# Kernel optimization log

Measured on AMD Instinct MI355X. Metric: run time of the kernel, lower is better.

## Reference

```python
import jax, jax.numpy as jnp
import numpy as np

GROUPS = 32
HEADS = 4
EPS_GN = 1e-5
EPS_DEN = 1e-6


def group_norm(x, gamma, beta):
    b, c, h, w = x.shape
    xg = x.reshape(b, GROUPS, (c // GROUPS) * h * w)
    mu = xg.mean(axis=-1, keepdims=True)
    var = xg.var(axis=-1, keepdims=True)
    xn = ((xg - mu) * jax.lax.rsqrt(var + EPS_GN)).reshape(b, c, h, w)
    return xn * gamma[None, :, None, None] + beta[None, :, None, None]


def setup_inputs() -> dict:
    key = jax.random.key(0)
    ks = jax.random.split(key, 4)
    b, c, h, w = 16, 256, 64, 64
    x = jax.random.normal(ks[0], (b, c, h, w), dtype=jnp.float32)
    gamma = jnp.ones((c,), jnp.float32)
    beta = jnp.zeros((c,), jnp.float32)
    w_qkv = jax.random.normal(ks[1], (3 * c, c), jnp.float32) * (1.0 / np.sqrt(c))
    b_qkv = jnp.zeros((3 * c,), jnp.float32)
    w_out = jax.random.normal(ks[2], (c, c), jnp.float32) * (1.0 / np.sqrt(c))
    b_out = jnp.zeros((c,), jnp.float32)
    return {"x": x, "gamma": gamma, "beta": beta, "w_qkv": w_qkv,
            "b_qkv": b_qkv, "w_out": w_out, "b_out": b_out}


def reference(x, gamma, beta, w_qkv, b_qkv, w_out, b_out):
    b, c, h, w = x.shape
    d = c // HEADS
    n = h * w
    xn = group_norm(x, gamma, beta)
    # 1x1 conv == channel GEMM: [b,3c,h,w]
    qkv = jnp.einsum('bchw,oc->bohw', xn, w_qkv) + b_qkv[None, :, None, None]
    q, k, v = jnp.split(qkv, 3, axis=1)
    # b (heads d) h w -> b heads d n
    q = q.reshape(b, HEADS, d, n)
    k = k.reshape(b, HEADS, d, n)
    v = v.reshape(b, HEADS, d, n)
    q = jax.nn.elu(q) + 1.0
    k = jax.nn.elu(k) + 1.0
    k_sum = k.sum(axis=-1)                                 # [b,H,d]
    kv = jnp.einsum('bhdn,bhen->bhde', k, v)               # [b,H,d,d]
    out = jnp.einsum('bhde,bhdn->bhen', kv, q)             # [b,H,d,n]
    denom = jnp.einsum('bhdn,bhd->bhn', q, k_sum)          # [b,H,n]
    out = out / (denom[:, :, None, :] + EPS_DEN)
    out = out.reshape(b, c, h, w)
    out = jnp.einsum('bchw,oc->bohw', out, w_out) + b_out[None, :, None, None]
    return out + x
```

## Files before the change

kernel.cpp:

```cpp
#include <hip/hip_runtime.h>
#include <stdint.h>

#define BATCH 16
#define CH    256
#define NSP   4096
#define NH    4
#define HD    64

typedef __attribute__((ext_vector_type(8))) short bf16x8;
typedef __attribute__((ext_vector_type(4))) float f32x4;
typedef __attribute__((ext_vector_type(4))) unsigned int u32x4;

__device__ __forceinline__ short f2bf(float f) {
    union { float f; unsigned u; } v; v.f = f;
    unsigned r = (v.u + 0x7fffu + ((v.u >> 16) & 1u)) >> 16;
    return (short)r;
}
__device__ __forceinline__ float bf2f(short s) {
    union { float f; unsigned u; } v; v.u = ((unsigned)(unsigned short)s) << 16;
    return v.f;
}

__global__ __launch_bounds__(256) void k_pre(
        const float* __restrict__ x, const float* __restrict__ wq, const float* __restrict__ wo,
        const float* __restrict__ gamma, const float* __restrict__ beta,
        float* __restrict__ sc_tab, float* __restrict__ sh_tab,
        short* __restrict__ wq_bf, short* __restrict__ wo_bf) {
    int bg = blockIdx.x;
    if (bg < 512) {
        const float4* p = (const float4*)(x + (size_t)bg * 32768);
        float s = 0.f, sq = 0.f;
        #pragma unroll 4
        for (int i = threadIdx.x; i < 8192; i += 256) {
            float4 v = p[i];
            s  += v.x + v.y + v.z + v.w;
            sq += v.x * v.x + v.y * v.y + v.z * v.z + v.w * v.w;
        }
        for (int off = 32; off; off >>= 1) { s += __shfl_down(s, off); sq += __shfl_down(sq, off); }
        __shared__ float ls[4], lq[4];
        int w = threadIdx.x >> 6;
        if ((threadIdx.x & 63) == 0) { ls[w] = s; lq[w] = sq; }
        __syncthreads();
        if (threadIdx.x == 0) {
            float S = ls[0] + ls[1] + ls[2] + ls[3];
            float Q = lq[0] + lq[1] + lq[2] + lq[3];
            float m = S / 32768.f;
            float var = Q / 32768.f - m * m;
            ls[0] = m; lq[0] = rsqrtf(var + 1e-5f);
        }
        __syncthreads();
        if (threadIdx.x < 8) {
            int b = bg >> 5, g = bg & 31, c = g * 8 + threadIdx.x;
            float r = lq[0], mm = ls[0];
            float sc = r * gamma[c];
            sc_tab[b * 256 + c] = sc;
            sh_tab[b * 256 + c] = beta[c] - mm * sc;
        }
    } else {
        int idx = ((bg - 512) * 256 + threadIdx.x) * 4;
        float4 v;
        short* dst;
        if (idx < 196608) { v = *(const float4*)(wq + idx); dst = wq_bf + idx; }
        else              { v = *(const float4*)(wo + (idx - 196608)); dst = wo_bf + (idx - 196608); }
        unsigned p0 = ((unsigned)(unsigned short)f2bf(v.x)) | (((unsigned)(unsigned short)f2bf(v.y)) << 16);
        unsigned p1 = ((unsigned)(unsigned short)f2bf(v.z)) | (((unsigned)(unsigned short)f2bf(v.w)) << 16);
        uint2 pk; pk.x = p0; pk.y = p1;
        *(uint2*)dst = pk;
    }
}

__global__ __launch_bounds__(256, 3) void k_gnqkv(
        const float* __restrict__ x,
        const float* __restrict__ sc_tab, const float* __restrict__ sh_tab,
        const short* __restrict__ wq_bf, const float* __restrict__ b_qkv,
        short* __restrict__ q_t, short* __restrict__ kvp_bf, float* __restrict__ ksp) {
    int b = blockIdx.y, nt = blockIdx.x;
    int n0 = nt * 64;
    __shared__ short Blds[64 * 264];
    __shared__ union UR {
        struct { short kst[64 * 72]; short vst[64 * 72]; } s;
        short cst[64 * 136];
    } R;
    int t = threadIdx.x, lane = t & 63, wv = t >> 6, lr = lane & 15, quad = lane >> 4;

    {
        const float* xb = x + (size_t)b * CH * NSP + n0;
        const float* scb = sc_tab + b * 256;
        const float* shb = sh_tab + b * 256;
        int m = t & 15, cq = t >> 4;
        float4 vv[16];
        float scA[16], shA[16];
        #pragma unroll
        for (int cb = 0; cb < 16; cb++) {
            int c = cb * 16 + cq;
            vv[cb] = *(const float4*)(xb + (size_t)c * NSP + m * 4);
            scA[cb] = scb[c]; shA[cb] = shb[c];
        }
        #pragma unroll
        for (int cb = 0; cb < 16; cb++) {
            int c = cb * 16 + cq;
            float va[4] = {vv[cb].x, vv[cb].y, vv[cb].z, vv[cb].w};
            #pragma unroll
            for (int j = 0; j < 4; j++) {
                int n = m * 4 + j;
                int cc = c ^ (((n >> 4) & 3) << 3);
                Blds[n * 264 + cc] = f2bf(va[j] * scA[cb] + shA[cb]);
            }
        }
    }
    __syncthreads();

    #pragma unroll 1
    for (int h = 0; h < 4; h++) {
        int br0 = (wv < 2 ? 256 : 512) + h * 64;
        int sub = (wv & 1) * 32;
        bf16x8 A0[8], A1[8];
        #pragma unroll
        for (int kk = 0; kk < 8; kk++) {
            A0[kk] = *(const bf16x8*)(wq_bf + (size_t)(br0 + sub + lr) * 256 + kk * 32 + quad * 8);
            A1[kk] = *(const bf16x8*)(wq_bf + (size_t)(br0 + sub + 16 + lr) * 256 + kk * 32 + quad * 8);
        }
        __builtin_amdgcn_sched_barrier(0);
        f32x4 acc[2][4] = {};
        #pragma unroll
        for (int kk = 0; kk < 8; kk++) {
            bf16x8 bfr[4];
            #pragma unroll
            for (int ni = 0; ni < 4; ni++) {
                int rr = ni * 16 + lr;
                bfr[ni] = *(const bf16x8*)(Blds + rr * 264 + ((kk * 32 + quad * 8) ^ (((rr >> 4) & 3) << 3)));
            }
            #pragma unroll
            for (int ni = 0; ni < 4; ni++) {
                acc[0][ni] = __builtin_amdgcn_mfma_f32_16x16x32_bf16(A0[kk], bfr[ni], acc[0][ni], 0, 0, 0);
                acc[1][ni] = __builtin_amdgcn_mfma_f32_16x16x32_bf16(A1[kk], bfr[ni], acc[1][ni], 0, 0, 0);
            }
        }
        __syncthreads();
        short* dst = (wv < 2) ? R.s.kst : R.s.vst;
        bool is_k = (wv < 2);
        #pragma unroll
        for (int mi = 0; mi < 2; mi++)
          #pragma unroll
          for (int ni = 0; ni < 4; ni++)
            #pragma unroll
            for (int r = 0; r < 4; r++) {
                int ol = sub + mi * 16 + quad * 4 + r;
                int nl = ni * 16 + lr;
                float v = acc[mi][ni][r] + b_qkv[br0 + ol];
                if (is_k) v = v > 0.f ? v + 1.f : __expf(v);
                dst[ol * 72 + nl] = f2bf(v);
            }
        __syncthreads();
        {
            int d = t >> 2, nq = (t & 3) * 16;
            float s = 0.f;
            #pragma unroll
            for (int j = 0; j < 16; j++) s += bf2f(R.s.kst[d * 72 + nq + j]);
            s += __shfl_down(s, 2);
            s += __shfl_down(s, 1);
            if ((t & 3) == 0) ksp[((size_t)(b * 4 + h) * 64 + nt) * 64 + d] = s;
        }
        f32x4 acc2[4] = {};
        #pragma unroll
        for (int kk = 0; kk < 64; kk += 32) {
            bf16x8 af = *(const bf16x8*)(R.s.vst + (wv * 16 + lr) * 72 + kk + quad * 8);
            bf16x8 bfk[4];
            #pragma unroll
            for (int ni = 0; ni < 4; ni++)
                bfk[ni] = *(const bf16x8*)(R.s.kst + (ni * 16 + lr) * 72 + kk + quad * 8);
            #pragma unroll
            for (int ni = 0; ni < 4; ni++)
                acc2[ni] = __builtin_amdgcn_mfma_f32_16x16x32_bf16(af, bfk[ni], acc2[ni], 0, 0, 0);
        }
        short* kvdst = kvp_bf + ((size_t)(b * 4 + h) * 64 + nt) * 4096;
        #pragma unroll
        for (int ni = 0; ni < 4; ni++)
            #pragma unroll
            for (int r = 0; r < 4; r++)
                kvdst[(wv * 16 + quad * 4 + r) * 64 + ni * 16 + lr] = f2bf(acc2[ni][r]);
    }

    #pragma unroll 1
    for (int mtq = 0; mtq < 2; mtq++) {
        int wm = wv * 32;
        bf16x8 A0[8], A1[8];
        #pragma unroll
        for (int kk = 0; kk < 8; kk++) {
            A0[kk] = *(const bf16x8*)(wq_bf + (size_t)(mtq * 128 + wm + lr) * 256 + kk * 32 + quad * 8);
            A1[kk] = *(const bf16x8*)(wq_bf + (size_t)(mtq * 128 + wm + 16 + lr) * 256 + kk * 32 + quad * 8);
        }
        __builtin_amdgcn_sched_barrier(0);
        f32x4 acc[2][4] = {};
        #pragma unroll
        for (int kk = 0; kk < 8; kk++) {
            bf16x8 bfr[4];
            #pragma unroll
            for (int ni = 0; ni < 4; ni++) {
                int rr = ni * 16 + lr;
                bfr[ni] = *(const bf16x8*)(Blds + rr * 264 + ((kk * 32 + quad * 8) ^ (((rr >> 4) & 3) << 3)));
            }
            #pragma unroll
            for (int ni = 0; ni < 4; ni++) {
                acc[0][ni] = __builtin_amdgcn_mfma_f32_16x16x32_bf16(A0[kk], bfr[ni], acc[0][ni], 0, 0, 0);
                acc[1][ni] = __builtin_amdgcn_mfma_f32_16x16x32_bf16(A1[kk], bfr[ni], acc[1][ni], 0, 0, 0);
            }
        }
        __syncthreads();
        #pragma unroll
        for (int mi = 0; mi < 2; mi++)
          #pragma unroll
          for (int ni = 0; ni < 4; ni++)
            #pragma unroll
            for (int r = 0; r < 4; r++) {
                int ol = wm + mi * 16 + quad * 4 + r;
                int nl = ni * 16 + lr;
                float v = acc[mi][ni][r] + b_qkv[mtq * 128 + ol];
                v = v > 0.f ? v + 1.f : __expf(v);
                R.cst[nl * 136 + ol] = f2bf(v);
            }
        __syncthreads();
        #pragma unroll
        for (int i = 0; i < 4; i++) {
            int ch = t + i * 256;
            int row = ch >> 4, o8 = (ch & 15) * 8;
            int hh = mtq * 2 + (o8 >> 6), d0 = o8 & 63;
            *(u32x4*)(q_t + ((size_t)(b * 4 + hh) * NSP + n0 + row) * HD + d0) =
                *(const u32x4*)(R.cst + row * 136 + o8);
        }
    }
}

__global__ __launch_bounds__(256) void k_kv_reduce(
        const short* __restrict__ kvp_bf, const float* __restrict__ ksp,
        short* __restrict__ kvT_bf, float* __restrict__ ksum_g) {
    int p = blockIdx.x, bh = blockIdx.y;
    int t = threadIdx.x, lane = t & 63, grp = t >> 6;
    int chunk = p * 64 + lane;
    const short* base = kvp_bf + (size_t)bh * 64 * 4096 + chunk * 8;
    float s[8] = {};
    for (int ntc = grp * 16; ntc < grp * 16 + 16; ntc++) {
        bf16x8 v = *(const bf16x8*)(base + (size_t)ntc * 4096);
        #pragma unroll
        for (int j = 0; j < 8; j++) s[j] += bf2f(v[j]);
    }
    __shared__ float red[4][64][8];
    if (grp) {
        #pragma unroll
        for (int j = 0; j < 8; j++) red[grp][lane][j] = s[j];
    }
    __syncthreads();
    if (grp == 0) {
        bf16x8 rv;
        #pragma unroll
        for (int j = 0; j < 8; j++) {
            float v = s[j] + red[1][lane][j] + red[2][lane][j] + red[3][lane][j];
            rv[j] = f2bf(v);
        }
        *(bf16x8*)(kvT_bf + (size_t)bh * 4096 + chunk * 8) = rv;
    }
    if (p == 0) {
        const float* kb = ksp + (size_t)bh * 64 * 64 + lane;
        float ss = 0.f;
        for (int ntc = grp * 16; ntc < grp * 16 + 16; ntc++) ss += kb[(size_t)ntc * 64];
        __syncthreads();
        red[grp][lane][0] = ss;
        __syncthreads();
        if (grp == 0) ksum_g[bh * 64 + lane] = ss + red[1][lane][0] + red[2][lane][0] + red[3][lane][0];
    }
}

__global__ __launch_bounds__(256, 3) void k_attn_out(
        const short* __restrict__ q_t, const short* __restrict__ kvT_bf,
        const float* __restrict__ ksum_g, const short* __restrict__ wo_bf,
        const float* __restrict__ b_out, const float* __restrict__ x,
        float* __restrict__ out) {
    int b = blockIdx.y, nt = blockIdx.x;
    int n0 = nt * 64;
    __shared__ short Battn[64 * 264];
    __shared__ short ql[64 * 72];
    __shared__ short kvl[64 * 72];
    __shared__ float dnp[4][64];
    int t = threadIdx.x, lane = t & 63, wv = t >> 6, lr = lane & 15, quad = lane >> 4;

    #pragma unroll 1
    for (int h = 0; h < 4; h++) {
        int bh = b * 4 + h;
        #pragma unroll
        for (int i = 0; i < 2; i++) {
            int ch = t + i * 256;
            int row = ch >> 3, dc = (ch & 7) * 8;
            *(u32x4*)(ql + row * 72 + dc) =
                *(const u32x4*)(q_t + ((size_t)bh * NSP + n0 + row) * HD + dc);
            *(u32x4*)(kvl + row * 72 + dc) =
                *(const u32x4*)(kvT_bf + (size_t)bh * 4096 + row * 64 + dc);
        }
        __syncthreads();
        {
            int n = t & 63, q0 = wv * 16;
            const float* ks = ksum_g + bh * 64 + q0;
            float s = 0.f;
            #pragma unroll
            for (int j = 0; j < 16; j += 8) {
                bf16x8 qv = *(const bf16x8*)(ql + n * 72 + q0 + j);
                #pragma unroll
                for (int u = 0; u < 8; u++) s += bf2f(qv[u]) * ks[j + u];
            }
            dnp[wv][n] = s;
        }
        f32x4 acc[4] = {};
        #pragma unroll
        for (int kk = 0; kk < 64; kk += 32) {
            bf16x8 af = *(const bf16x8*)(ql + (wv * 16 + lr) * 72 + kk + quad * 8);
            bf16x8 bfr[4];
            #pragma unroll
            for (int ni = 0; ni < 4; ni++)
                bfr[ni] = *(const bf16x8*)(kvl + (ni * 16 + lr) * 72 + kk + quad * 8);
            #pragma unroll
            for (int ni = 0; ni < 4; ni++)
                acc[ni] = __builtin_amdgcn_mfma_f32_16x16x32_bf16(af, bfr[ni], acc[ni], 0, 0, 0);
        }
        __syncthreads();
        float dn[4];
        #pragma unroll
        for (int r = 0; r < 4; r++) {
            int n = wv * 16 + quad * 4 + r;
            dn[r] = 1.f / (dnp[0][n] + dnp[1][n] + dnp[2][n] + dnp[3][n] + 1e-6f);
        }
        #pragma unroll
        for (int ni = 0; ni < 4; ni++)
            #pragma unroll
            for (int r = 0; r < 4; r++) {
                int n = wv * 16 + quad * 4 + r;
                Battn[n * 264 + h * 64 + ni * 16 + lr] = f2bf(acc[ni][r] * dn[r]);
            }
        __syncthreads();
    }

    #pragma unroll 1
    for (int p = 0; p < 2; p++) {
        int rbase = p * 128 + wv * 32;
        bf16x8 A0[8], A1[8];
        #pragma unroll
        for (int kk = 0; kk < 8; kk++) {
            A0[kk] = *(const bf16x8*)(wo_bf + (size_t)(rbase + lr) * 256 + kk * 32 + quad * 8);
            A1[kk] = *(const bf16x8*)(wo_bf + (size_t)(rbase + 16 + lr) * 256 + kk * 32 + quad * 8);
        }
        __builtin_amdgcn_sched_barrier(0);
        f32x4 acc[2][4] = {};
        #pragma unroll
        for (int kk = 0; kk < 8; kk++) {
            bf16x8 bfr[4];
            #pragma unroll
            for (int ni = 0; ni < 4; ni++)
                bfr[ni] = *(const bf16x8*)(Battn + (ni * 16 + lr) * 264 + kk * 32 + quad * 8);
            #pragma unroll
            for (int ni = 0; ni < 4; ni++) {
                acc[0][ni] = __builtin_amdgcn_mfma_f32_16x16x32_bf16(A0[kk], bfr[ni], acc[0][ni], 0, 0, 0);
                acc[1][ni] = __builtin_amdgcn_mfma_f32_16x16x32_bf16(A1[kk], bfr[ni], acc[1][ni], 0, 0, 0);
            }
        }
        #pragma unroll
        for (int mi = 0; mi < 2; mi++)
          #pragma unroll
          for (int ni = 0; ni < 4; ni++)
            #pragma unroll
            for (int r = 0; r < 4; r++) {
                int o = rbase + mi * 16 + quad * 4 + r;
                int nl = ni * 16 + lr;
                size_t idx = ((size_t)b * CH + o) * NSP + n0 + nl;
                out[idx] = acc[mi][ni][r] + b_out[o] + x[idx];
            }
    }
}

extern "C" void kernel_launch(void* const* d_in, const int* in_sizes, int n_in,
                              void* d_out, int out_size, void* d_ws, size_t ws_size,
                              hipStream_t stream) {
    const float* x     = (const float*)d_in[0];
    const float* gamma = (const float*)d_in[1];
    const float* beta  = (const float*)d_in[2];
    const float* w_qkv = (const float*)d_in[3];
    const float* b_qkv = (const float*)d_in[4];
    const float* w_out = (const float*)d_in[5];
    const float* b_out = (const float*)d_in[6];
    float* out = (float*)d_out;

    char* ws = (char*)d_ws;
    size_t off = 0;
    float* sc_tab = (float*)(ws + off); off += (size_t)16 * 256 * 4;
    float* sh_tab = (float*)(ws + off); off += (size_t)16 * 256 * 4;
    short* wq_bf  = (short*)(ws + off); off += (size_t)768 * 256 * 2;
    short* wo_bf  = (short*)(ws + off); off += (size_t)256 * 256 * 2;
    short* q_t    = (short*)(ws + off); off += (size_t)BATCH * NSP * CH * 2;
    short* kvp_bf = (short*)(ws + off); off += (size_t)64 * 64 * 4096 * 2;
    float* ksp    = (float*)(ws + off); off += (size_t)64 * 64 * 64 * 4;
    short* kvT_bf = (short*)(ws + off); off += (size_t)64 * 4096 * 2;
    float* ksum_g = (float*)(ws + off); off += (size_t)64 * 64 * 4;

    if (ws_size < off) return;

    k_pre<<<768, 256, 0, stream>>>(x, w_qkv, w_out, gamma, beta, sc_tab, sh_tab, wq_bf, wo_bf);
    k_gnqkv<<<dim3(64, 16), 256, 0, stream>>>(x, sc_tab, sh_tab, wq_bf, b_qkv, q_t, kvp_bf, ksp);
    k_kv_reduce<<<dim3(2 * 4, 64), 256, 0, stream>>>(kvp_bf, ksp, kvT_bf, ksum_g);
    k_attn_out<<<dim3(64, 16), 256, 0, stream>>>(q_t, kvT_bf, ksum_g, wo_bf, b_out, x, out);
}
```

Baseline: 271.9 us.

## Double block size to 512 threads and split MFMA tiles across eight waves

Both main kernels move from 256 to 512 threads per block, so eight waves share each 64-column tile and each wave computes half as many N subtiles. Weight fragments are now loaded per k-step instead of all preloaded into registers, and the ksum reduction runs on waves 4-7 while waves 0-3 compute the per-tile KV product. The Q projection is done in one pass that writes into the reused Blds buffer, which removes the second LDS staging region. The aim is to cut register pressure and raise occupancy and latency hiding, but each wave now reloads the weights and there is more barrier overhead per block.

```diff
diff --git a/kernel.cpp b/kernel.cpp
--- a/kernel.cpp
+++ b/kernel.cpp
@@ -69,7 +69,7 @@
     }
 }
 
-__global__ __launch_bounds__(256, 3) void k_gnqkv(
+__global__ __launch_bounds__(512, 4) void k_gnqkv(
         const float* __restrict__ x,
         const float* __restrict__ sc_tab, const float* __restrict__ sh_tab,
         const short* __restrict__ wq_bf, const float* __restrict__ b_qkv,
@@ -77,10 +77,8 @@
     int b = blockIdx.y, nt = blockIdx.x;
     int n0 = nt * 64;
     __shared__ short Blds[64 * 264];
-    __shared__ union UR {
-        struct { short kst[64 * 72]; short vst[64 * 72]; } s;
-        short cst[64 * 136];
-    } R;
+    __shared__ short kst[64 * 72];
+    __shared__ short vst[64 * 72];
     int t = threadIdx.x, lane = t & 63, wv = t >> 6, lr = lane & 15, quad = lane >> 4;
 
     {
@@ -88,23 +86,17 @@
         const float* scb = sc_tab + b * 256;
         const float* shb = sh_tab + b * 256;
         int m = t & 15, cq = t >> 4;
-        float4 vv[16];
-        float scA[16], shA[16];
-        #pragma unroll
-        for (int cb = 0; cb < 16; cb++) {
-            int c = cb * 16 + cq;
-            vv[cb] = *(const float4*)(xb + (size_t)c * NSP + m * 4);
-            scA[cb] = scb[c]; shA[cb] = shb[c];
-        }
-        #pragma unroll
-        for (int cb = 0; cb < 16; cb++) {
-            int c = cb * 16 + cq;
-            float va[4] = {vv[cb].x, vv[cb].y, vv[cb].z, vv[cb].w};
+        #pragma unroll 2
+        for (int cb = 0; cb < 8; cb++) {
+            int c = cb * 32 + cq;
+            float sc = scb[c], sh = shb[c];
+            float4 v = *(const float4*)(xb + (size_t)c * NSP + m * 4);
+            float va[4] = {v.x, v.y, v.z, v.w};
             #pragma unroll
             for (int j = 0; j < 4; j++) {
                 int n = m * 4 + j;
                 int cc = c ^ (((n >> 4) & 3) << 3);
-                Blds[n * 264 + cc] = f2bf(va[j] * scA[cb] + shA[cb]);
+                Blds[n * 264 + cc] = f2bf(va[j] * sc + sh);
             }
         }
     }
@@ -112,121 +104,117 @@
 
     #pragma unroll 1
     for (int h = 0; h < 4; h++) {
-        int br0 = (wv < 2 ? 256 : 512) + h * 64;
-        int sub = (wv & 1) * 32;
-        bf16x8 A0[8], A1[8];
+        int rb = (wv & 3) * 32;
+        bool is_k = rb < 64;
+        int gbase = (is_k ? 256 : 512) + h * 64;
+        int lrow0 = is_k ? rb : rb - 64;
+        int nih = (wv >> 2) * 2;
+        f32x4 acc[2][2] = {};
         #pragma unroll
         for (int kk = 0; kk < 8; kk++) {
-            A0[kk] = *(const bf16x8*)(wq_bf + (size_t)(br0 + sub + lr) * 256 + kk * 32 + quad * 8);
-            A1[kk] = *(const bf16x8*)(wq_bf + (size_t)(br0 + sub + 16 + lr) * 256 + kk * 32 + quad * 8);
-        }
-        __builtin_amdgcn_sched_barrier(0);
-        f32x4 acc[2][4] = {};
-        #pragma unroll
-        for (int kk = 0; kk < 8; kk++) {
-            bf16x8 bfr[4];
-            #pragma unroll
-            for (int ni = 0; ni < 4; ni++) {
-                int rr = ni * 16 + lr;
-                bfr[ni] = *(const bf16x8*)(Blds + rr * 264 + ((kk * 32 + quad * 8) ^ (((rr >> 4) & 3) << 3)));
-            }
-            #pragma unroll
-            for (int ni = 0; ni < 4; ni++) {
-                acc[0][ni] = __builtin_amdgcn_mfma_f32_16x16x32_bf16(A0[kk], bfr[ni], acc[0][ni], 0, 0, 0);
-                acc[1][ni] = __builtin_amdgcn_mfma_f32_16x16x32_bf16(A1[kk], bfr[ni], acc[1][ni], 0, 0, 0);
-            }
-        }
-        __syncthreads();
-        short* dst = (wv < 2) ? R.s.kst : R.s.vst;
-        bool is_k = (wv < 2);
+            bf16x8 a0 = *(const bf16x8*)(wq_bf + (size_t)(gbase + lrow0 + lr) * 256 + kk * 32 + quad * 8);
+            bf16x8 a1 = *(const bf16x8*)(wq_bf + (size_t)(gbase + lrow0 + 16 + lr) * 256 + kk * 32 + quad * 8);
+            bf16x8 bfr[2];
+            #pragma unroll
+            for (int nj = 0; nj < 2; nj++) {
+                int rr = (nih + nj) * 16 + lr;
+                bfr[nj] = *(const bf16x8*)(Blds + rr * 264 + ((kk * 32 + quad * 8) ^ (((rr >> 4) & 3) << 3)));
+            }
+            #pragma unroll
+            for (int nj = 0; nj < 2; nj++) {
+                acc[0][nj] = __builtin_amdgcn_mfma_f32_16x16x32_bf16(a0, bfr[nj], acc[0][nj], 0, 0, 0);
+                acc[1][nj] = __builtin_amdgcn_mfma_f32_16x16x32_bf16(a1, bfr[nj], acc[1][nj], 0, 0, 0);
+            }
+        }
+        __syncthreads();
+        short* dst = is_k ? kst : vst;
         #pragma unroll
         for (int mi = 0; mi < 2; mi++)
           #pragma unroll
-          for (int ni = 0; ni < 4; ni++)
+          for (int nj = 0; nj < 2; nj++)
             #pragma unroll
             for (int r = 0; r < 4; r++) {
-                int ol = sub + mi * 16 + quad * 4 + r;
-                int nl = ni * 16 + lr;
-                float v = acc[mi][ni][r] + b_qkv[br0 + ol];
+                int ol = lrow0 + mi * 16 + quad * 4 + r;
+                int nl = (nih + nj) * 16 + lr;
+                float v = acc[mi][nj][r] + b_qkv[gbase + ol];
                 if (is_k) v = v > 0.f ? v + 1.f : __expf(v);
                 dst[ol * 72 + nl] = f2bf(v);
             }
         __syncthreads();
-        {
-            int d = t >> 2, nq = (t & 3) * 16;
+        if (wv < 4) {
+            f32x4 acc2[4] = {};
+            #pragma unroll
+            for (int kk = 0; kk < 64; kk += 32) {
+                bf16x8 af = *(const bf16x8*)(vst + (wv * 16 + lr) * 72 + kk + quad * 8);
+                bf16x8 bfk[4];
+                #pragma unroll
+                for (int ni = 0; ni < 4; ni++)
+                    bfk[ni] = *(const bf16x8*)(kst + (ni * 16 + lr) * 72 + kk + quad * 8);
+                #pragma unroll
+                for (int ni = 0; ni < 4; ni++)
+                    acc2[ni] = __builtin_amdgcn_mfma_f32_16x16x32_bf16(af, bfk[ni], acc2[ni], 0, 0, 0);
+            }
+            short* kvdst = kvp_bf + ((size_t)(b * 4 + h) * 64 + nt) * 4096;
+            #pragma unroll
+            for (int ni = 0; ni < 4; ni++)
+                #pragma unroll
+                for (int r = 0; r < 4; r++)
+                    kvdst[(wv * 16 + quad * 4 + r) * 64 + ni * 16 + lr] = f2bf(acc2[ni][r]);
+        } else {
+            int tt = t - 256;
+            int d = tt >> 2, nq = (tt & 3) * 16;
             float s = 0.f;
             #pragma unroll
-            for (int j = 0; j < 16; j++) s += bf2f(R.s.kst[d * 72 + nq + j]);
+            for (int j = 0; j < 16; j++) s += bf2f(kst[d * 72 + nq + j]);
             s += __shfl_down(s, 2);
             s += __shfl_down(s, 1);
-            if ((t & 3) == 0) ksp[((size_t)(b * 4 + h) * 64 + nt) * 64 + d] = s;
-        }
-        f32x4 acc2[4] = {};
-        #pragma unroll
-        for (int kk = 0; kk < 64; kk += 32) {
-            bf16x8 af = *(const bf16x8*)(R.s.vst + (wv * 16 + lr) * 72 + kk + quad * 8);
-            bf16x8 bfk[4];
-            #pragma unroll
-            for (int ni = 0; ni < 4; ni++)
-                bfk[ni] = *(const bf16x8*)(R.s.kst + (ni * 16 + lr) * 72 + kk + quad * 8);
-            #pragma unroll
-            for (int ni = 0; ni < 4; ni++)
-                acc2[ni] = __builtin_amdgcn_mfma_f32_16x16x32_bf16(af, bfk[ni], acc2[ni], 0, 0, 0);
-        }
-        short* kvdst = kvp_bf + ((size_t)(b * 4 + h) * 64 + nt) * 4096;
-        #pragma unroll
-        for (int ni = 0; ni < 4; ni++)
-            #pragma unroll
-            for (int r = 0; r < 4; r++)
-                kvdst[(wv * 16 + quad * 4 + r) * 64 + ni * 16 + lr] = f2bf(acc2[ni][r]);
-    }
-
-    #pragma unroll 1
-    for (int mtq = 0; mtq < 2; mtq++) {
-        int wm = wv * 32;
-        bf16x8 A0[8], A1[8];
+            if ((tt & 3) == 0) ksp[((size_t)(b * 4 + h) * 64 + nt) * 64 + d] = s;
+        }
+    }
+
+    {
+        int r0 = (wv & 3) * 64, nih = (wv >> 2) * 2;
+        f32x4 acc[4][2] = {};
         #pragma unroll
         for (int kk = 0; kk < 8; kk++) {
-            A0[kk] = *(const bf16x8*)(wq_bf + (size_t)(mtq * 128 + wm + lr) * 256 + kk * 32 + quad * 8);
-            A1[kk] = *(const bf16x8*)(wq_bf + (size_t)(mtq * 128 + wm + 16 + lr) * 256 + kk * 32 + quad * 8);
-        }
-        __builtin_amdgcn_sched_barrier(0);
-        f32x4 acc[2][4] = {};
-        #pragma unroll
-        for (int kk = 0; kk < 8; kk++) {
-            bf16x8 bfr[4];
-            #pragma unroll
-            for (int ni = 0; ni < 4; ni++) {
-                int rr = ni * 16 + lr;
-                bfr[ni] = *(const bf16x8*)(Blds + rr * 264 + ((kk * 32 + quad * 8) ^ (((rr >> 4) & 3) << 3)));
-            }
-            #pragma unroll
-            for (int ni = 0; ni < 4; ni++) {
-                acc[0][ni] = __builtin_amdgcn_mfma_f32_16x16x32_bf16(A0[kk], bfr[ni], acc[0][ni], 0, 0, 0);
-                acc[1][ni] = __builtin_amdgcn_mfma_f32_16x16x32_bf16(A1[kk], bfr[ni], acc[1][ni], 0, 0, 0);
-            }
-        }
-        __syncthreads();
-        #pragma unroll
-        for (int mi = 0; mi < 2; mi++)
+            bf16x8 A[4];
+            #pragma unroll
+            for (int mi = 0; mi < 4; mi++)
+                A[mi] = *(const bf16x8*)(wq_bf + (size_t)(r0 + mi * 16 + lr) * 256 + kk * 32 + quad * 8);
+            bf16x8 bfr[2];
+            #pragma unroll
+            for (int nj = 0; nj < 2; nj++) {
+                int rr = (nih + nj) * 16 + lr;
+                bfr[nj] = *(const bf16x8*)(Blds + rr * 264 + ((kk * 32 + quad * 8) ^ (((rr >> 4) & 3) << 3)));
+            }
+            #pragma unroll
+            for (int mi = 0; mi < 4; mi++)
+                #pragma unroll
+                for (int nj = 0; nj < 2; nj++)
+                    acc[mi][nj] = __builtin_amdgcn_mfma_f32_16x16x32_bf16(A[mi], bfr[nj], acc[mi][nj], 0, 0, 0);
+        }
+        __syncthreads();
+        #pragma unroll
+        for (int mi = 0; mi < 4; mi++)
           #pragma unroll
-          for (int ni = 0; ni < 4; ni++)
+          for (int nj = 0; nj < 2; nj++)
             #pragma unroll
             for (int r = 0; r < 4; r++) {
-                int ol = wm + mi * 16 + quad * 4 + r;
-                int nl = ni * 16 + lr;
-                float v = acc[mi][ni][r] + b_qkv[mtq * 128 + ol];
+                int ol = r0 + mi * 16 + quad * 4 + r;
+                int nl = (nih + nj) * 16 + lr;
+                float v = acc[mi][nj][r] + b_qkv[ol];
                 v = v > 0.f ? v + 1.f : __expf(v);
-                R.cst[nl * 136 + ol] = f2bf(v);
+                Blds[nl * 264 + ol] = f2bf(v);
             }
         __syncthreads();
         #pragma unroll
         for (int i = 0; i < 4; i++) {
-            int ch = t + i * 256;
-            int row = ch >> 4, o8 = (ch & 15) * 8;
-            int hh = mtq * 2 + (o8 >> 6), d0 = o8 & 63;
+            int ch = t + i * 512;
+            int row = ch >> 5;
+            int o8 = (ch & 31) * 8;
+            int hh = o8 >> 6, d0 = o8 & 63;
             *(u32x4*)(q_t + ((size_t)(b * 4 + hh) * NSP + n0 + row) * HD + d0) =
-                *(const u32x4*)(R.cst + row * 136 + o8);
+                *(const u32x4*)(Blds + row * 264 + o8);
         }
     }
 }
@@ -270,7 +258,7 @@
     }
 }
 
-__global__ __launch_bounds__(256, 3) void k_attn_out(
+__global__ __launch_bounds__(512, 4) void k_attn_out(
         const short* __restrict__ q_t, const short* __restrict__ kvT_bf,
         const float* __restrict__ ksum_g, const short* __restrict__ wo_bf,
         const float* __restrict__ b_out, const float* __restrict__ x,
@@ -280,16 +268,14 @@
     __shared__ short Battn[64 * 264];
     __shared__ short ql[64 * 72];
     __shared__ short kvl[64 * 72];
-    __shared__ float dnp[4][64];
+    __shared__ float dnp[8][64];
     int t = threadIdx.x, lane = t & 63, wv = t >> 6, lr = lane & 15, quad = lane >> 4;
 
     #pragma unroll 1
     for (int h = 0; h < 4; h++) {
         int bh = b * 4 + h;
-        #pragma unroll
-        for (int i = 0; i < 2; i++) {
-            int ch = t + i * 256;
-            int row = ch >> 3, dc = (ch & 7) * 8;
+        {
+            int row = t >> 3, dc = (t & 7) * 8;
             *(u32x4*)(ql + row * 72 + dc) =
                 *(const u32x4*)(q_t + ((size_t)bh * NSP + n0 + row) * HD + dc);
             *(u32x4*)(kvl + row * 72 + dc) =
@@ -297,79 +283,73 @@
         }
         __syncthreads();
         {
-            int n = t & 63, q0 = wv * 16;
-            const float* ks = ksum_g + bh * 64 + q0;
+            int n = t & 63;
+            bf16x8 qv = *(const bf16x8*)(ql + n * 72 + wv * 8);
+            const float* ks = ksum_g + bh * 64 + wv * 8;
             float s = 0.f;
             #pragma unroll
-            for (int j = 0; j < 16; j += 8) {
-                bf16x8 qv = *(const bf16x8*)(ql + n * 72 + q0 + j);
-                #pragma unroll
-                for (int u = 0; u < 8; u++) s += bf2f(qv[u]) * ks[j + u];
-            }
+            for (int u = 0; u < 8; u++) s += bf2f(qv[u]) * ks[u];
             dnp[wv][n] = s;
         }
-        f32x4 acc[4] = {};
+        int nr = (wv & 3) * 16, nih = (wv >> 2) * 2;
+        f32x4 acc[2] = {};
         #pragma unroll
         for (int kk = 0; kk < 64; kk += 32) {
-            bf16x8 af = *(const bf16x8*)(ql + (wv * 16 + lr) * 72 + kk + quad * 8);
-            bf16x8 bfr[4];
-            #pragma unroll
-            for (int ni = 0; ni < 4; ni++)
-                bfr[ni] = *(const bf16x8*)(kvl + (ni * 16 + lr) * 72 + kk + quad * 8);
-            #pragma unroll
-            for (int ni = 0; ni < 4; ni++)
-                acc[ni] = __builtin_amdgcn_mfma_f32_16x16x32_bf16(af, bfr[ni], acc[ni], 0, 0, 0);
+            bf16x8 af = *(const bf16x8*)(ql + (nr + lr) * 72 + kk + quad * 8);
+            #pragma unroll
+            for (int nj = 0; nj < 2; nj++) {
+                bf16x8 bfr = *(const bf16x8*)(kvl + ((nih + nj) * 16 + lr) * 72 + kk + quad * 8);
+                acc[nj] = __builtin_amdgcn_mfma_f32_16x16x32_bf16(af, bfr, acc[nj], 0, 0, 0);
+            }
         }
         __syncthreads();
         float dn[4];
         #pragma unroll
         for (int r = 0; r < 4; r++) {
-            int n = wv * 16 + quad * 4 + r;
-            dn[r] = 1.f / (dnp[0][n] + dnp[1][n] + dnp[2][n] + dnp[3][n] + 1e-6f);
-        }
-        #pragma unroll
-        for (int ni = 0; ni < 4; ni++)
+            int n = nr + quad * 4 + r;
+            float s = dnp[0][n] + dnp[1][n] + dnp[2][n] + dnp[3][n]
+                    + dnp[4][n] + dnp[5][n] + dnp[6][n] + dnp[7][n];
+            dn[r] = 1.f / (s + 1e-6f);
+        }
+        #pragma unroll
+        for (int nj = 0; nj < 2; nj++)
             #pragma unroll
             for (int r = 0; r < 4; r++) {
-                int n = wv * 16 + quad * 4 + r;
-                Battn[n * 264 + h * 64 + ni * 16 + lr] = f2bf(acc[ni][r] * dn[r]);
-            }
-        __syncthreads();
-    }
-
-    #pragma unroll 1
-    for (int p = 0; p < 2; p++) {
-        int rbase = p * 128 + wv * 32;
-        bf16x8 A0[8], A1[8];
+                int n = nr + quad * 4 + r;
+                Battn[n * 264 + h * 64 + (nih + nj) * 16 + lr] = f2bf(acc[nj][r] * dn[r]);
+            }
+    }
+    __syncthreads();
+
+    {
+        int r0 = (wv & 3) * 64, nih = (wv >> 2) * 2;
+        f32x4 acc[4][2] = {};
         #pragma unroll
         for (int kk = 0; kk < 8; kk++) {
-            A0[kk] = *(const bf16x8*)(wo_bf + (size_t)(rbase + lr) * 256 + kk * 32 + quad * 8);
-            A1[kk] = *(const bf16x8*)(wo_bf + (size_t)(rbase + 16 + lr) * 256 + kk * 32 + quad * 8);
-        }
-        __builtin_amdgcn_sched_barrier(0);
-        f32x4 acc[2][4] = {};
-        #pragma unroll
-        for (int kk = 0; kk < 8; kk++) {
-            bf16x8 bfr[4];
-            #pragma unroll
-            for (int ni = 0; ni < 4; ni++)
-                bfr[ni] = *(const bf16x8*)(Battn + (ni * 16 + lr) * 264 + kk * 32 + quad * 8);
-            #pragma unroll
-            for (int ni = 0; ni < 4; ni++) {
-                acc[0][ni] = __builtin_amdgcn_mfma_f32_16x16x32_bf16(A0[kk], bfr[ni], acc[0][ni], 0, 0, 0);
-                acc[1][ni] = __builtin_amdgcn_mfma_f32_16x16x32_bf16(A1[kk], bfr[ni], acc[1][ni], 0, 0, 0);
-            }
-        }
-        #pragma unroll
-        for (int mi = 0; mi < 2; mi++)
+            bf16x8 A[4];
+            #pragma unroll
+            for (int mi = 0; mi < 4; mi++)
+                A[mi] = *(const bf16x8*)(wo_bf + (size_t)(r0 + mi * 16 + lr) * 256 + kk * 32 + quad * 8);
+            bf16x8 bfr[2];
+            #pragma unroll
+            for (int nj = 0; nj < 2; nj++)
+                bfr[nj] = *(const bf16x8*)(Battn + ((nih + nj) * 16 + lr) * 264 + kk * 32 + quad * 8);
+            #pragma unroll
+            for (int mi = 0; mi < 4; mi++)
+                #pragma unroll
+                for (int nj = 0; nj < 2; nj++)
+                    acc[mi][nj] = __builtin_amdgcn_mfma_f32_16x16x32_bf16(A[mi], bfr[nj], acc[mi][nj], 0, 0, 0);
+        }
+        #pragma unroll
+        for (int mi = 0; mi < 4; mi++)
           #pragma unroll
-          for (int ni = 0; ni < 4; ni++)
+          for (int nj = 0; nj < 2; nj++)
             #pragma unroll
             for (int r = 0; r < 4; r++) {
-                int o = rbase + mi * 16 + quad * 4 + r;
-                int nl = ni * 16 + lr;
+                int o = r0 + mi * 16 + quad * 4 + r;
+                int nl = (nih + nj) * 16 + lr;
                 size_t idx = ((size_t)b * CH + o) * NSP + n0 + nl;
-                out[idx] = acc[mi][ni][r] + b_out[o] + x[idx];
+                out[idx] = acc[mi][nj][r] + b_out[o] + x[idx];
             }
     }
 }
@@ -401,7 +381,7 @@
     if (ws_size < off) return;
 
     k_pre<<<768, 256, 0, stream>>>(x, w_qkv, w_out, gamma, beta, sc_tab, sh_tab, wq_bf, wo_bf);
-    k_gnqkv<<<dim3(64, 16), 256, 0, stream>>>(x, sc_tab, sh_tab, wq_bf, b_qkv, q_t, kvp_bf, ksp);
-    k_kv_reduce<<<dim3(2 * 4, 64), 256, 0, stream>>>(kvp_bf, ksp, kvT_bf, ksum_g);
-    k_attn_out<<<dim3(64, 16), 256, 0, stream>>>(q_t, kvT_bf, ksum_g, wo_bf, b_out, x, out);
-}
+    k_gnqkv<<<dim3(64, 16), 512, 0, stream>>>(x, sc_tab, sh_tab, wq_bf, b_qkv, q_t, kvp_bf, ksp);
+    k_kv_reduce<<<dim3(8, 64), 256, 0, stream>>>(kvp_bf, ksp, kvT_bf, ksum_g);
+    k_attn_out<<<dim3(64, 16), 512, 0, stream>>>(q_t, kvT_bf, ksum_g, wo_bf, b_out, x, out);
+}
```

Result: slower. 293.2 us (+7.8%).
